# Kernel optimization log

Hardware: AMD Instinct MI355X
Metric: run time of the kernel (lower is better)

Reference implementation:

```python
import jax, jax.numpy as jnp
import numpy as np

D_IN = 4096
NUM_LATENTS = 65536
GROUP_DIM = 64
GROUP_MUL = 4
IN_GROUPS = D_IN // GROUP_DIM      # 64
OUT_GROUPS = NUM_LATENTS // GROUP_DIM  # 1024
TOKENS = 2048


def setup_inputs() -> dict:
    key = jax.random.key(0)
    k1, k2, k3, k4, k5 = jax.random.split(key, 5)
    x = jax.random.normal(k1, (TOKENS, D_IN), dtype=jnp.float32)
    # nn.Linear default init ~ U(-1/sqrt(d), 1/sqrt(d)); scale randn similarly for stability
    s = 1.0 / np.sqrt(D_IN)
    pre_w = jax.random.normal(k2, (D_IN, D_IN), dtype=jnp.float32) * s
    pre_b = jax.random.normal(k3, (D_IN,), dtype=jnp.float32) * s
    inner = jax.random.normal(k4, (GROUP_MUL, IN_GROUPS, GROUP_DIM, GROUP_DIM), dtype=jnp.float32)
    outer = jax.random.normal(k5, (OUT_GROUPS, GROUP_MUL, IN_GROUPS), dtype=jnp.float32)
    return {"x": x, "pre_w": pre_w, "pre_b": pre_b, "inner": inner, "outer": outer}


def reference(x, pre_w, pre_b, inner, outer):
    # pre: dense linear, x @ W^T + b  -> (tokens, d_in)
    h = x @ pre_w.T + pre_b
    # unflatten last dim into (in_groups, group_dim)
    h = h.reshape(h.shape[0], IN_GROUPS, GROUP_DIM)  # (b, i, x)
    # block-diagonal mix: (b,i,x) x (m,i,x,y) -> (b,m,i,y)
    t = jnp.einsum('bix,mixy->bmiy', h, inner)
    # low-rank outer combine: (b,m,i,y) x (o,m,i) -> (b,o,y)
    out = jnp.einsum('bmiy,omi->boy', t, outer)
    # flatten (o, y) -> num_latents; note: module's _bias is unused in forward
    return out.reshape(out.shape[0], NUM_LATENTS)
```

## Files before the change

kernel.cpp:

```cpp
#include <hip/hip_runtime.h>
#include <hip/hip_bf16.h>
#include <stdint.h>

#define D_IN 4096
#define TOKENS 2048
#define NUM_LATENTS 65536
#define GROUP_DIM 64
#define GROUP_MUL 4
#define IN_GROUPS 64
#define OUT_GROUPS 1024
#define KMID 256

typedef __attribute__((ext_vector_type(8))) short short8;
typedef __attribute__((ext_vector_type(4))) float f32x4;

struct alignas(8)  US4 { unsigned short v[4]; };

#define FLAT_BLOCKS 24832

__device__ inline unsigned short f2bf(float f) {
    union { float f; unsigned u; } w{f};
    unsigned r = w.u + 0x7fffu + ((w.u >> 16) & 1u);
    return (unsigned short)(r >> 16);
}

__device__ inline void gload_lds16(const void* g, void* l) {
    __builtin_amdgcn_global_load_lds(
        (const __attribute__((address_space(1))) void*)g,
        (__attribute__((address_space(3))) void*)l, 16, 0, 0);
}

__device__ inline int SWZ(int y, int k) {
    return ((y << 9) + (k << 1)) ^ ((((y & 7) ^ ((y >> 3) & 7)) << 4));
}

__global__ __launch_bounds__(256) void cvt_all(
    const float* __restrict__ w, const float* __restrict__ x,
    const float* __restrict__ outer, const float* __restrict__ inner,
    unsigned short* __restrict__ w_bf, unsigned short* __restrict__ x_bf,
    unsigned short* __restrict__ o_bf, unsigned short* __restrict__ it_bf) {
    __shared__ float tl[64][65];
    int blk = blockIdx.x;
    const int tid = threadIdx.x;
    if (blk >= FLAT_BLOCKS) {
        blk -= FLAT_BLOCKS;
        const float* src = inner + (size_t)blk * 4096;
        #pragma unroll
        for (int p = 0; p < 4; ++p) {
            int idx = p * 1024 + tid * 4;
            int xx = idx >> 6, y = idx & 63;
            f32x4 v = *(const f32x4*)(src + idx);
            #pragma unroll
            for (int j = 0; j < 4; ++j) tl[xx][y + j] = v[j];
        }
        __syncthreads();
        unsigned short* dst = it_bf + (size_t)blk * 4096;
        #pragma unroll
        for (int p = 0; p < 4; ++p) {
            int idx = p * 1024 + tid * 4;
            int y = idx >> 6, x0 = idx & 63;
            US4 o;
            #pragma unroll
            for (int j = 0; j < 4; ++j) o.v[j] = f2bf(tl[x0 + j][y]);
            *(US4*)(dst + y * 64 + (x0 ^ ((y & 7) << 3))) = o;
        }
        return;
    }
    int s = blk * 256 + tid;
    if (s < 4194304) {
        f32x4 v = *(const f32x4*)(w + (size_t)s * 4);
        US4 o;
        #pragma unroll
        for (int j = 0; j < 4; ++j) o.v[j] = f2bf(v[j]);
        *(US4*)(w_bf + (size_t)s * 4) = o;
    } else if (s < 6291456) {
        int t = s - 4194304;
        f32x4 v = *(const f32x4*)(x + (size_t)t * 4);
        US4 o;
        #pragma unroll
        for (int j = 0; j < 4; ++j) o.v[j] = f2bf(v[j]);
        *(US4*)(x_bf + (size_t)t * 4) = o;
    } else {
        int t0 = (s - 6291456) * 4;
        int o = t0 >> 8, r = t0 & 255, m = r >> 6, i = r & 63;
        f32x4 v = *(const f32x4*)(outer + t0);
        #pragma unroll
        for (int j = 0; j < 4; ++j)
            o_bf[(o << 8) + (i + j) * 4 + m] = f2bf(v[j]);
    }
}

__global__ __launch_bounds__(256, 2) void gemm_fused(
    const unsigned short* __restrict__ A,
    const unsigned short* __restrict__ B,
    const float* __restrict__ bias,
    const unsigned short* __restrict__ IT,
    unsigned short* __restrict__ T)
{
    __shared__ unsigned short smem[40960];
    unsigned short* inn = smem + 32768;

    const int tid = threadIdx.x;
    const int lane = tid & 63;
    const int w = tid >> 6;
    const int wm = w >> 1, wn = w & 1;
    int bx = blockIdx.x;
    bx = (bx & 7) * 64 + (bx >> 3);
    const int m0 = (bx & 15) * 128;
    const int n0 = (bx >> 4) * 128;
    const int i0 = n0 >> 6;

    const int lr = lane & 15;
    const int hi = lane >> 4;
    const int lk = hi * 8;

    f32x4 acc[4][4] = {};

    auto STAGE = [&](int buf, int k0) {
        #pragma unroll
        for (int c = 0; c < 4; ++c) {
            int f = c * 2048 + tid * 8;
            int r = f >> 6;
            int colsw = ((((f >> 3) & 7) ^ (r & 7)) << 3);
            gload_lds16(A + (size_t)(m0 + r) * D_IN + k0 + colsw, smem + buf * 16384 + f);
            gload_lds16(B + (size_t)(n0 + r) * D_IN + k0 + colsw, smem + buf * 16384 + 8192 + f);
        }
    };
    auto COMPUTE = [&](int buf) {
        const unsigned short* as = smem + buf * 16384;
        const unsigned short* bs = as + 8192;
        #pragma unroll
        for (int kk = 0; kk < 2; ++kk) {
            short8 a[4], b[4];
            #pragma unroll
            for (int mi = 0; mi < 4; ++mi) {
                int row = wm * 64 + mi * 16 + lr;
                a[mi] = *(const short8*)(as + (row << 6) + ((((kk << 2) + hi) ^ (lr & 7)) << 3));
            }
            #pragma unroll
            for (int ni = 0; ni < 4; ++ni) {
                int row = wn * 64 + ni * 16 + lr;
                b[ni] = *(const short8*)(bs + (row << 6) + ((((kk << 2) + hi) ^ (lr & 7)) << 3));
            }
            __builtin_amdgcn_s_setprio(1);
            #pragma unroll
            for (int mi = 0; mi < 4; ++mi)
                #pragma unroll
                for (int ni = 0; ni < 4; ++ni)
                    acc[mi][ni] = __builtin_amdgcn_mfma_f32_16x16x32_bf16(b[ni], a[mi], acc[mi][ni], 0, 0, 0);
            __builtin_amdgcn_s_setprio(0);
        }
    };

    STAGE(0, 0);
    #pragma unroll 1
    for (int t = 0; t < 64; ++t) {
        asm volatile("s_waitcnt vmcnt(0)" ::: "memory");
        __builtin_amdgcn_s_barrier();
        __builtin_amdgcn_sched_barrier(0);
        if (t < 63) STAGE((t + 1) & 1, (t + 1) * 64);
        COMPUTE(t & 1);
        __builtin_amdgcn_sched_barrier(0);
    }

    #pragma unroll
    for (int ni = 0; ni < 4; ++ni) {
        int col0 = wn * 64 + ni * 16 + hi * 4;
        f32x4 bv = *(const f32x4*)(bias + n0 + col0);
        #pragma unroll
        for (int mi = 0; mi < 4; ++mi) {
            int tok = wm * 64 + mi * 16 + lr;
            US4 o;
            #pragma unroll
            for (int j = 0; j < 4; ++j) o.v[j] = f2bf(acc[mi][ni][j] + bv[j]);
            *(US4*)(smem + tok * 128 + (col0 ^ ((tok & 7) << 3))) = o;
        }
    }

    for (int m = 0; m < 4; ++m) {
        #pragma unroll
        for (int c = 0; c < 4; ++c) {
            int e = c * 2048 + tid * 8;
            int i_loc = e >> 12, rem = e & 4095;
            gload_lds16(IT + ((size_t)(m * 64 + i0 + i_loc) << 12) + rem, inn + e);
        }
        asm volatile("s_waitcnt vmcnt(0)" ::: "memory");
        __syncthreads();

        f32x4 acc2[4][4] = {};
        #pragma unroll
        for (int kk = 0; kk < 2; ++kk) {
            short8 a[4], b2[4];
            #pragma unroll
            for (int mi = 0; mi < 4; ++mi) {
                int tok = wm * 64 + mi * 16 + lr;
                a[mi] = *(const short8*)(smem + tok * 128 + ((wn * 64 + kk * 32 + lk) ^ ((tok & 7) << 3)));
            }
            #pragma unroll
            for (int ni = 0; ni < 4; ++ni) {
                int y = ni * 16 + lr;
                b2[ni] = *(const short8*)(inn + wn * 4096 + y * 64 + ((kk * 32 + lk) ^ ((y & 7) << 3)));
            }
            #pragma unroll
            for (int mi = 0; mi < 4; ++mi)
                #pragma unroll
                for (int ni = 0; ni < 4; ++ni)
                    acc2[mi][ni] = __builtin_amdgcn_mfma_f32_16x16x32_bf16(b2[ni], a[mi], acc2[mi][ni], 0, 0, 0);
        }

        const int kp = (i0 + wn) * 4 + m;
        #pragma unroll
        for (int mi = 0; mi < 4; ++mi) {
            int tok = m0 + wm * 64 + mi * 16 + lr;
            unsigned short* trow = T + ((size_t)tok * KMID + kp) * 64;
            #pragma unroll
            for (int ni = 0; ni < 4; ++ni) {
                int y0 = ni * 16 + hi * 4;
                US4 o;
                #pragma unroll
                for (int j = 0; j < 4; ++j) o.v[j] = f2bf(acc2[mi][ni][j]);
                *(US4*)(trow + y0) = o;
            }
        }
        __syncthreads();
    }
}

__global__ __launch_bounds__(256, 2) void stage3(
    const unsigned short* __restrict__ T,
    const unsigned short* __restrict__ Ob,
    float* __restrict__ out)
{
    __shared__ char ts[32768];
    const int tid = threadIdx.x;
    const int lane = tid & 63;
    const int w = tid >> 6;
    const int bx = blockIdx.x;
    const int xcd = bx & 7, j = bx >> 3;
    const int b = xcd * 256 + (j >> 1);
    const int half = j & 1;
    const int lr = lane & 15;
    const int hi = lane >> 4;

    {
        const unsigned short* src = T + (size_t)b * (KMID * 64);
        #pragma unroll
        for (int c = 0; c < 8; ++c) {
            int e = c * 2048 + tid * 8;
            int k = e >> 6, y = e & 63;
            short8 v = __builtin_nontemporal_load((const short8*)(src + e));
            #pragma unroll
            for (int jj = 0; jj < 8; ++jj)
                *(unsigned short*)(ts + SWZ(y + jj, k)) = (unsigned short)v[jj];
        }
    }
    __syncthreads();

    const int o_base = half * 512 + w * 128;
    f32x4 acc[4][8] = {};
    for (int kt = 0; kt < 8; ++kt) {
        short8 tf[4], of[8];
        #pragma unroll
        for (int ni = 0; ni < 4; ++ni)
            tf[ni] = *(const short8*)(ts + SWZ(ni * 16 + lr, kt * 32 + hi * 8));
        #pragma unroll
        for (int mi = 0; mi < 8; ++mi)
            of[mi] = *(const short8*)(Ob + ((size_t)(o_base + mi * 16 + lr) << 8) + kt * 32 + hi * 8);
        #pragma unroll
        for (int ni = 0; ni < 4; ++ni)
            #pragma unroll
            for (int mi = 0; mi < 8; ++mi)
                acc[ni][mi] = __builtin_amdgcn_mfma_f32_16x16x32_bf16(tf[ni], of[mi], acc[ni][mi], 0, 0, 0);
    }

    float* ob = out + (size_t)b * NUM_LATENTS;
    #pragma unroll
    for (int ni = 0; ni < 4; ++ni) {
        #pragma unroll
        for (int mi = 0; mi < 8; ++mi) {
            int o = o_base + mi * 16 + lr;
            int y = ni * 16 + hi * 4;
            __builtin_nontemporal_store(acc[ni][mi], (f32x4*)(ob + (o << 6) + y));
        }
    }
}

extern "C" void kernel_launch(void* const* d_in, const int* in_sizes, int n_in,
                              void* d_out, int out_size, void* d_ws, size_t ws_size,
                              hipStream_t stream) {
    const float* x     = (const float*)d_in[0];
    const float* pre_w = (const float*)d_in[1];
    const float* pre_b = (const float*)d_in[2];
    const float* inner = (const float*)d_in[3];
    const float* outer = (const float*)d_in[4];
    float* out = (float*)d_out;

    char* ws = (char*)d_ws;
    unsigned short* x_bf = (unsigned short*)ws;  ws += (size_t)TOKENS * D_IN * 2;
    unsigned short* w_bf = (unsigned short*)ws;  ws += (size_t)D_IN * D_IN * 2;
    unsigned short* o_bf = (unsigned short*)ws;  ws += (size_t)OUT_GROUPS * KMID * 2;
    unsigned short* t_bf = (unsigned short*)ws;  ws += (size_t)TOKENS * KMID * 64 * 2;
    unsigned short* it_bf = (unsigned short*)ws; ws += (size_t)GROUP_MUL * IN_GROUPS * 64 * 64 * 2;

    cvt_all<<<FLAT_BLOCKS + GROUP_MUL * IN_GROUPS, 256, 0, stream>>>(
        pre_w, x, outer, inner, w_bf, x_bf, o_bf, it_bf);

    gemm_fused<<<512, 256, 0, stream>>>(x_bf, w_bf, pre_b, it_bf, t_bf);
    stage3<<<4096, 256, 0, stream>>>(t_bf, o_bf, out);
}
```

Baseline: 350.3 us.

## Split-K the pre-GEMM, move block-diagonal mix into separate kernel, reshape stage3

Splits the dense pre-GEMM into two K halves over 1024 blocks with a smaller 32-wide K tile and a triple-buffered load pipeline, writing fp32 partials to workspace. A new h2t kernel sums the partials, adds the bias, converts to bf16 and runs the block-diagonal mix, prefetching the next inner-weight slab while storing results. stage3 now uses 512-thread blocks, each covering half of the y dimension of one token. The goal is more resident blocks and better latency hiding on 256 CUs, at the cost of an extra 64 MB of fp32 partial traffic and one more kernel launch.

```diff
diff --git a/kernel.cpp b/kernel.cpp
--- a/kernel.cpp
+++ b/kernel.cpp
@@ -5,10 +5,8 @@
 #define D_IN 4096
 #define TOKENS 2048
 #define NUM_LATENTS 65536
-#define GROUP_DIM 64
 #define GROUP_MUL 4
 #define IN_GROUPS 64
-#define OUT_GROUPS 1024
 #define KMID 256
 
 typedef __attribute__((ext_vector_type(8))) short short8;
@@ -90,110 +88,143 @@
     }
 }
 
-__global__ __launch_bounds__(256, 2) void gemm_fused(
+__global__ __launch_bounds__(256, 4) void gemm_splitk(
     const unsigned short* __restrict__ A,
     const unsigned short* __restrict__ B,
-    const float* __restrict__ bias,
-    const unsigned short* __restrict__ IT,
-    unsigned short* __restrict__ T)
+    float* __restrict__ P)
 {
-    __shared__ unsigned short smem[40960];
-    unsigned short* inn = smem + 32768;
+    __shared__ unsigned short smem[24576];
 
     const int tid = threadIdx.x;
     const int lane = tid & 63;
     const int w = tid >> 6;
     const int wm = w >> 1, wn = w & 1;
     int bx = blockIdx.x;
-    bx = (bx & 7) * 64 + (bx >> 3);
-    const int m0 = (bx & 15) * 128;
-    const int n0 = (bx >> 4) * 128;
+    const int logical = (bx & 7) * 128 + (bx >> 3);
+    const int ks = logical & 1;
+    const int tile = logical >> 1;
+    const int m0 = (tile & 15) * 128;
+    const int n0 = (tile >> 4) * 128;
+    const int kb = ks * 2048;
+
+    const int lr = lane & 15;
+    const int hi = lane >> 4;
+
+    f32x4 acc[4][4] = {};
+
+    auto STAGE = [&](int buf, int k0) {
+        #pragma unroll
+        for (int c = 0; c < 2; ++c) {
+            int f = c * 2048 + tid * 8;
+            int r = f >> 5;
+            int colsw = ((((f >> 3) & 3) ^ (r & 3)) << 3);
+            gload_lds16(A + (size_t)(m0 + r) * D_IN + k0 + colsw, smem + buf * 8192 + f);
+            gload_lds16(B + (size_t)(n0 + r) * D_IN + k0 + colsw, smem + buf * 8192 + 4096 + f);
+        }
+    };
+    auto COMPUTE = [&](int buf) {
+        const unsigned short* as = smem + buf * 8192;
+        const unsigned short* bs = as + 4096;
+        short8 a[4], b[4];
+        #pragma unroll
+        for (int mi = 0; mi < 4; ++mi) {
+            int row = wm * 64 + mi * 16 + lr;
+            a[mi] = *(const short8*)(as + (row << 5) + ((hi ^ (row & 3)) << 3));
+        }
+        #pragma unroll
+        for (int ni = 0; ni < 4; ++ni) {
+            int row = wn * 64 + ni * 16 + lr;
+            b[ni] = *(const short8*)(bs + (row << 5) + ((hi ^ (row & 3)) << 3));
+        }
+        __builtin_amdgcn_s_setprio(1);
+        #pragma unroll
+        for (int mi = 0; mi < 4; ++mi)
+            #pragma unroll
+            for (int ni = 0; ni < 4; ++ni)
+                acc[mi][ni] = __builtin_amdgcn_mfma_f32_16x16x32_bf16(b[ni], a[mi], acc[mi][ni], 0, 0, 0);
+        __builtin_amdgcn_s_setprio(0);
+    };
+
+    STAGE(0, kb);
+    STAGE(1, kb + 32);
+    int bcur = 0, bn2 = 2;
+    #pragma unroll 1
+    for (int t = 0; t < 64; ++t) {
+        if (t < 63) { asm volatile("s_waitcnt vmcnt(4)" ::: "memory"); }
+        else        { asm volatile("s_waitcnt vmcnt(0)" ::: "memory"); }
+        __builtin_amdgcn_s_barrier();
+        __builtin_amdgcn_sched_barrier(0);
+        if (t < 62) STAGE(bn2, kb + (t + 2) * 32);
+        COMPUTE(bcur);
+        __builtin_amdgcn_sched_barrier(0);
+        bcur = (bcur == 2) ? 0 : bcur + 1;
+        bn2  = (bn2 == 2) ? 0 : bn2 + 1;
+    }
+
+    float* pb = P + (size_t)ks * 8388608;
+    #pragma unroll
+    for (int ni = 0; ni < 4; ++ni) {
+        int col0 = n0 + wn * 64 + ni * 16 + hi * 4;
+        #pragma unroll
+        for (int mi = 0; mi < 4; ++mi) {
+            int tok = m0 + wm * 64 + mi * 16 + lr;
+            __builtin_nontemporal_store(acc[mi][ni], (f32x4*)(pb + (size_t)tok * 4096 + col0));
+        }
+    }
+}
+
+__global__ __launch_bounds__(256) void h2t(
+    const float* __restrict__ P,
+    const float* __restrict__ bias,
+    const unsigned short* __restrict__ IT,
+    unsigned short* __restrict__ T)
+{
+    __shared__ unsigned short smem[16384];
+    unsigned short* inn = smem + 8192;
+    const int tid = threadIdx.x;
+    const int lane = tid & 63;
+    const int w = tid >> 6;
+    const int wm = w >> 1, wn = w & 1;
+    const int bx = blockIdx.x;
+    const int m0 = (bx & 31) * 64;
+    const int n0 = (bx >> 5) * 128;
     const int i0 = n0 >> 6;
 
     const int lr = lane & 15;
     const int hi = lane >> 4;
     const int lk = hi * 8;
 
-    f32x4 acc[4][4] = {};
-
-    auto STAGE = [&](int buf, int k0) {
-        #pragma unroll
-        for (int c = 0; c < 4; ++c) {
-            int f = c * 2048 + tid * 8;
-            int r = f >> 6;
-            int colsw = ((((f >> 3) & 7) ^ (r & 7)) << 3);
-            gload_lds16(A + (size_t)(m0 + r) * D_IN + k0 + colsw, smem + buf * 16384 + f);
-            gload_lds16(B + (size_t)(n0 + r) * D_IN + k0 + colsw, smem + buf * 16384 + 8192 + f);
-        }
-    };
-    auto COMPUTE = [&](int buf) {
-        const unsigned short* as = smem + buf * 16384;
-        const unsigned short* bs = as + 8192;
-        #pragma unroll
-        for (int kk = 0; kk < 2; ++kk) {
-            short8 a[4], b[4];
-            #pragma unroll
-            for (int mi = 0; mi < 4; ++mi) {
-                int row = wm * 64 + mi * 16 + lr;
-                a[mi] = *(const short8*)(as + (row << 6) + ((((kk << 2) + hi) ^ (lr & 7)) << 3));
-            }
-            #pragma unroll
-            for (int ni = 0; ni < 4; ++ni) {
-                int row = wn * 64 + ni * 16 + lr;
-                b[ni] = *(const short8*)(bs + (row << 6) + ((((kk << 2) + hi) ^ (lr & 7)) << 3));
-            }
-            __builtin_amdgcn_s_setprio(1);
-            #pragma unroll
-            for (int mi = 0; mi < 4; ++mi)
-                #pragma unroll
-                for (int ni = 0; ni < 4; ++ni)
-                    acc[mi][ni] = __builtin_amdgcn_mfma_f32_16x16x32_bf16(b[ni], a[mi], acc[mi][ni], 0, 0, 0);
-            __builtin_amdgcn_s_setprio(0);
-        }
-    };
-
-    STAGE(0, 0);
-    #pragma unroll 1
-    for (int t = 0; t < 64; ++t) {
-        asm volatile("s_waitcnt vmcnt(0)" ::: "memory");
-        __builtin_amdgcn_s_barrier();
-        __builtin_amdgcn_sched_barrier(0);
-        if (t < 63) STAGE((t + 1) & 1, (t + 1) * 64);
-        COMPUTE(t & 1);
-        __builtin_amdgcn_sched_barrier(0);
-    }
-
     #pragma unroll
-    for (int ni = 0; ni < 4; ++ni) {
-        int col0 = wn * 64 + ni * 16 + hi * 4;
-        f32x4 bv = *(const f32x4*)(bias + n0 + col0);
-        #pragma unroll
-        for (int mi = 0; mi < 4; ++mi) {
-            int tok = wm * 64 + mi * 16 + lr;
-            US4 o;
-            #pragma unroll
-            for (int j = 0; j < 4; ++j) o.v[j] = f2bf(acc[mi][ni][j] + bv[j]);
-            *(US4*)(smem + tok * 128 + (col0 ^ ((tok & 7) << 3))) = o;
-        }
+    for (int c = 0; c < 4; ++c) {
+        int e = c * 2048 + tid * 8;
+        int i_l = e >> 12, rem = e & 4095;
+        gload_lds16(IT + ((size_t)(i0 + i_l) << 12) + rem, inn + e);
+    }
+
+    #pragma unroll
+    for (int it = 0; it < 8; ++it) {
+        int idx = it * 1024 + tid * 4;
+        int r = idx >> 7, c = idx & 127;
+        f32x4 p0 = __builtin_nontemporal_load((const f32x4*)(P + (size_t)(m0 + r) * 4096 + n0 + c));
+        f32x4 p1 = __builtin_nontemporal_load((const f32x4*)(P + 8388608 + (size_t)(m0 + r) * 4096 + n0 + c));
+        f32x4 bv = *(const f32x4*)(bias + n0 + c);
+        US4 o;
+        #pragma unroll
+        for (int j = 0; j < 4; ++j) o.v[j] = f2bf(p0[j] + p1[j] + bv[j]);
+        *(US4*)(smem + r * 128 + (c ^ ((r & 7) << 3))) = o;
     }
 
     for (int m = 0; m < 4; ++m) {
-        #pragma unroll
-        for (int c = 0; c < 4; ++c) {
-            int e = c * 2048 + tid * 8;
-            int i_loc = e >> 12, rem = e & 4095;
-            gload_lds16(IT + ((size_t)(m * 64 + i0 + i_loc) << 12) + rem, inn + e);
-        }
         asm volatile("s_waitcnt vmcnt(0)" ::: "memory");
         __syncthreads();
 
-        f32x4 acc2[4][4] = {};
+        f32x4 acc2[2][4] = {};
         #pragma unroll
         for (int kk = 0; kk < 2; ++kk) {
-            short8 a[4], b2[4];
-            #pragma unroll
-            for (int mi = 0; mi < 4; ++mi) {
-                int tok = wm * 64 + mi * 16 + lr;
+            short8 a[2], b2[4];
+            #pragma unroll
+            for (int mi = 0; mi < 2; ++mi) {
+                int tok = wm * 32 + mi * 16 + lr;
                 a[mi] = *(const short8*)(smem + tok * 128 + ((wn * 64 + kk * 32 + lk) ^ ((tok & 7) << 3)));
             }
             #pragma unroll
@@ -202,7 +233,7 @@
                 b2[ni] = *(const short8*)(inn + wn * 4096 + y * 64 + ((kk * 32 + lk) ^ ((y & 7) << 3)));
             }
             #pragma unroll
-            for (int mi = 0; mi < 4; ++mi)
+            for (int mi = 0; mi < 2; ++mi)
                 #pragma unroll
                 for (int ni = 0; ni < 4; ++ni)
                     acc2[mi][ni] = __builtin_amdgcn_mfma_f32_16x16x32_bf16(b2[ni], a[mi], acc2[mi][ni], 0, 0, 0);
@@ -210,8 +241,8 @@
 
         const int kp = (i0 + wn) * 4 + m;
         #pragma unroll
-        for (int mi = 0; mi < 4; ++mi) {
-            int tok = m0 + wm * 64 + mi * 16 + lr;
+        for (int mi = 0; mi < 2; ++mi) {
+            int tok = m0 + wm * 32 + mi * 16 + lr;
             unsigned short* trow = T + ((size_t)tok * KMID + kp) * 64;
             #pragma unroll
             for (int ni = 0; ni < 4; ++ni) {
@@ -223,59 +254,63 @@
             }
         }
         __syncthreads();
-    }
-}
-
-__global__ __launch_bounds__(256, 2) void stage3(
+        if (m < 3) {
+            #pragma unroll
+            for (int c = 0; c < 4; ++c) {
+                int e = c * 2048 + tid * 8;
+                int i_l = e >> 12, rem = e & 4095;
+                gload_lds16(IT + ((size_t)((m + 1) * 64 + i0 + i_l) << 12) + rem, inn + e);
+            }
+        }
+    }
+}
+
+__global__ __launch_bounds__(512, 4) void stage3(
     const unsigned short* __restrict__ T,
     const unsigned short* __restrict__ Ob,
     float* __restrict__ out)
 {
-    __shared__ char ts[32768];
+    __shared__ char ts[16384];
     const int tid = threadIdx.x;
     const int lane = tid & 63;
     const int w = tid >> 6;
     const int bx = blockIdx.x;
-    const int xcd = bx & 7, j = bx >> 3;
-    const int b = xcd * 256 + (j >> 1);
-    const int half = j & 1;
+    const int logical = (bx & 7) * 512 + (bx >> 3);
+    const int b = logical >> 1;
+    const int yh = logical & 1;
     const int lr = lane & 15;
     const int hi = lane >> 4;
 
     {
-        const unsigned short* src = T + (size_t)b * (KMID * 64);
-        #pragma unroll
-        for (int c = 0; c < 8; ++c) {
-            int e = c * 2048 + tid * 8;
-            int k = e >> 6, y = e & 63;
-            short8 v = __builtin_nontemporal_load((const short8*)(src + e));
+        const unsigned short* src = T + (size_t)b * (KMID * 64) + yh * 32;
+        #pragma unroll
+        for (int j2 = 0; j2 < 2; ++j2) {
+            int e = tid * 16 + j2 * 8;
+            int k = e >> 5, yl = e & 31;
+            short8 v = __builtin_nontemporal_load((const short8*)(src + k * 64 + yl));
             #pragma unroll
             for (int jj = 0; jj < 8; ++jj)
-                *(unsigned short*)(ts + SWZ(y + jj, k)) = (unsigned short)v[jj];
+                *(unsigned short*)(ts + SWZ(yl + jj, k)) = (unsigned short)v[jj];
         }
     }
     __syncthreads();
 
-    const int o_base = half * 512 + w * 128;
-    f32x4 acc[4][8] = {};
+    const int o_base = w * 128;
+    f32x4 acc[2][8] = {};
     for (int kt = 0; kt < 8; ++kt) {
-        short8 tf[4], of[8];
-        #pragma unroll
-        for (int ni = 0; ni < 4; ++ni)
-            tf[ni] = *(const short8*)(ts + SWZ(ni * 16 + lr, kt * 32 + hi * 8));
-        #pragma unroll
-        for (int mi = 0; mi < 8; ++mi)
-            of[mi] = *(const short8*)(Ob + ((size_t)(o_base + mi * 16 + lr) << 8) + kt * 32 + hi * 8);
-        #pragma unroll
-        for (int ni = 0; ni < 4; ++ni)
-            #pragma unroll
-            for (int mi = 0; mi < 8; ++mi)
-                acc[ni][mi] = __builtin_amdgcn_mfma_f32_16x16x32_bf16(tf[ni], of[mi], acc[ni][mi], 0, 0, 0);
-    }
-
-    float* ob = out + (size_t)b * NUM_LATENTS;
+        short8 tf0 = *(const short8*)(ts + SWZ(lr, kt * 32 + hi * 8));
+        short8 tf1 = *(const short8*)(ts + SWZ(16 + lr, kt * 32 + hi * 8));
+        #pragma unroll
+        for (int mi = 0; mi < 8; ++mi) {
+            short8 of = *(const short8*)(Ob + ((size_t)(o_base + mi * 16 + lr) << 8) + kt * 32 + hi * 8);
+            acc[0][mi] = __builtin_amdgcn_mfma_f32_16x16x32_bf16(tf0, of, acc[0][mi], 0, 0, 0);
+            acc[1][mi] = __builtin_amdgcn_mfma_f32_16x16x32_bf16(tf1, of, acc[1][mi], 0, 0, 0);
+        }
+    }
+
+    float* ob = out + (size_t)b * NUM_LATENTS + yh * 32;
     #pragma unroll
-    for (int ni = 0; ni < 4; ++ni) {
+    for (int ni = 0; ni < 2; ++ni) {
         #pragma unroll
         for (int mi = 0; mi < 8; ++mi) {
             int o = o_base + mi * 16 + lr;
@@ -296,15 +331,17 @@
     float* out = (float*)d_out;
 
     char* ws = (char*)d_ws;
+    float* part = (float*)ws;                    ws += (size_t)2 * TOKENS * D_IN * 4;
     unsigned short* x_bf = (unsigned short*)ws;  ws += (size_t)TOKENS * D_IN * 2;
     unsigned short* w_bf = (unsigned short*)ws;  ws += (size_t)D_IN * D_IN * 2;
-    unsigned short* o_bf = (unsigned short*)ws;  ws += (size_t)OUT_GROUPS * KMID * 2;
+    unsigned short* o_bf = (unsigned short*)ws;  ws += (size_t)1024 * KMID * 2;
     unsigned short* t_bf = (unsigned short*)ws;  ws += (size_t)TOKENS * KMID * 64 * 2;
     unsigned short* it_bf = (unsigned short*)ws; ws += (size_t)GROUP_MUL * IN_GROUPS * 64 * 64 * 2;
 
     cvt_all<<<FLAT_BLOCKS + GROUP_MUL * IN_GROUPS, 256, 0, stream>>>(
         pre_w, x, outer, inner, w_bf, x_bf, o_bf, it_bf);
 
-    gemm_fused<<<512, 256, 0, stream>>>(x_bf, w_bf, pre_b, it_bf, t_bf);
-    stage3<<<4096, 256, 0, stream>>>(t_bf, o_bf, out);
-}
+    gemm_splitk<<<1024, 256, 0, stream>>>(x_bf, w_bf, part);
+    h2t<<<1024, 256, 0, stream>>>(part, pre_b, it_bf, t_bf);
+    stage3<<<4096, 512, 0, stream>>>(t_bf, o_bf, out);
+}
```

Result: slower. 469.1 us (+33.9%).
